# Kernel optimization log

Measured on AMD Instinct MI355X. Metric: run time of the kernel, lower is better.

Reference implementation:

```python
import jax, jax.numpy as jnp
import numpy as np


def _conv1x1(x, w, b):
    # x: (B, C, H, W), w: (O, C), b: (O,)  -> (B, O, H, W)
    return jnp.einsum('oc,bchw->bohw', w, x) + b[None, :, None, None]


def _branch(xq, xkv, wq, bq, wk, bk, wv, bv):
    B, C, H, W = xq.shape
    N = H * W
    q = _conv1x1(xq, wq, bq).reshape(B, -1, N)   # (B, d, N)
    k = _conv1x1(xkv, wk, bk).reshape(B, -1, N)  # (B, d, N)
    v = _conv1x1(xkv, wv, bv).reshape(B, C, N)   # (B, C, N)
    energy = jnp.einsum('bdi,bdj->bij', q, k)    # (B, N, N), no scale (as in source)
    attn = jax.nn.softmax(energy, axis=-1)
    out = jnp.einsum('bcj,bij->bci', v, attn)    # bmm(v, attn^T)
    return out.reshape(B, C, H, W)


def setup_inputs() -> dict:
    key = jax.random.key(0)
    ks = jax.random.split(key, 16)
    B, C, H, W = 4, 256, 64, 64
    d = C // 8
    s_in = 0.02
    inp = {
        'x1': jax.random.normal(ks[0], (B, C, H, W), jnp.float32),
        'x2': jax.random.normal(ks[1], (B, C, H, W), jnp.float32),
        'wq1': jax.random.normal(ks[2], (d, C), jnp.float32) * s_in,
        'bq1': jnp.zeros((d,), jnp.float32),
        'wk1': jax.random.normal(ks[3], (d, C), jnp.float32) * s_in,
        'bk1': jnp.zeros((d,), jnp.float32),
        'wv1': jax.random.normal(ks[4], (C, C), jnp.float32) * s_in,
        'bv1': jnp.zeros((C,), jnp.float32),
        'wq2': jax.random.normal(ks[5], (d, C), jnp.float32) * s_in,
        'bq2': jnp.zeros((d,), jnp.float32),
        'wk2': jax.random.normal(ks[6], (d, C), jnp.float32) * s_in,
        'bk2': jnp.zeros((d,), jnp.float32),
        'wv2': jax.random.normal(ks[7], (C, C), jnp.float32) * s_in,
        'bv2': jnp.zeros((C,), jnp.float32),
    }
    return inp


def reference(x1, x2, wq1, bq1, wk1, bk1, wv1, bv1, wq2, bq2, wk2, bk2, wv2, bv2):
    out1 = _branch(x1, x2, wq1, bq1, wk1, bk1, wv1, bv1)
    out2 = _branch(x1, x2, wq2, bq2, wk2, bk2, wv2, bv2)
    return x1 + x2 + out1 + out2
```

## Files before the change

kernel.cpp:

```cpp
#include <hip/hip_runtime.h>

#define N_TOK 4096
#define C_DIM 256
#define D_DIM 32

typedef float f32x4 __attribute__((ext_vector_type(4)));
typedef short short8 __attribute__((ext_vector_type(8)));
typedef unsigned short u16;

__device__ __forceinline__ u16 f2bf(float f) {
    unsigned int u = __builtin_bit_cast(unsigned int, f);
    u += 0x7fffu + ((u >> 16) & 1u);
    return (u16)(u >> 16);
}
__device__ __forceinline__ u16 f2bf_fast(float f) {
    return (u16)((__builtin_bit_cast(unsigned int, f) + 0x8000u) >> 16);
}
__device__ __forceinline__ float bf2f(u16 h) {
    unsigned int u = ((unsigned int)h) << 16;
    return __builtin_bit_cast(float, u);
}
__device__ __forceinline__ float exp2_fast(float x) {
#if __has_builtin(__builtin_amdgcn_exp2f)
    return __builtin_amdgcn_exp2f(x);
#else
    return exp2f(x);
#endif
}

__global__ __launch_bounds__(256) void qk_proj(
    const float* __restrict__ x1, const float* __restrict__ x2,
    const float* __restrict__ wq1, const float* __restrict__ bq1,
    const float* __restrict__ wk1, const float* __restrict__ bk1,
    const float* __restrict__ wq2, const float* __restrict__ bq2,
    const float* __restrict__ wk2, const float* __restrict__ bk2,
    u16* __restrict__ wsQ, u16* __restrict__ wsK)
{
    __shared__ float w_lds[32 * 256];
    const int ib = blockIdx.x;
    const int comb = blockIdx.y;
    const int b = comb & 3;
    const int branch = (comb >> 2) & 1;
    const int qk = comb >> 3;

    const float* x = qk ? x2 : x1;
    const float* w; const float* bias; u16* dst;
    if (qk == 0) { w = branch ? wq2 : wq1; bias = branch ? bq2 : bq1; dst = wsQ; }
    else         { w = branch ? wk2 : wk1; bias = branch ? bk2 : bk1; dst = wsK; }
    const int slice = branch * 4 + b;
    dst += (size_t)slice * N_TOK * D_DIM;
    const float osc = (qk == 0) ? 1.44269504088896341f : 1.0f;

    const int tid = threadIdx.x;
    for (int t = tid; t < 32 * 256; t += 256) w_lds[t] = w[t];
    __syncthreads();

    const int il = tid & 63;
    const int db = tid >> 6;
    const float* xc = x + (size_t)b * C_DIM * N_TOK + ib * 64 + il;

    float acc[8] = {0.f,0.f,0.f,0.f,0.f,0.f,0.f,0.f};
    for (int c4 = 0; c4 < 256; c4 += 4) {
        const float xv0 = xc[(size_t)(c4 + 0) * N_TOK];
        const float xv1 = xc[(size_t)(c4 + 1) * N_TOK];
        const float xv2 = xc[(size_t)(c4 + 2) * N_TOK];
        const float xv3 = xc[(size_t)(c4 + 3) * N_TOK];
#pragma unroll
        for (int mm = 0; mm < 8; ++mm) {
            const float4 wv = *(const float4*)&w_lds[(db * 8 + mm) * 256 + c4];
            acc[mm] += xv0 * wv.x + xv1 * wv.y + xv2 * wv.z + xv3 * wv.w;
        }
    }
    short8 pack;
#pragma unroll
    for (int mm = 0; mm < 8; ++mm)
        pack[mm] = (short)f2bf((acc[mm] + bias[db * 8 + mm]) * osc);
    *(short8*)(dst + (size_t)(ib * 64 + il) * D_DIM + db * 8) = pack;
}

__device__ __forceinline__ void stage_xt(u16* xtb, const float* xb, int ks,
                                         int wave, int lane)
{
    const int j  = (wave & 1) * 64 + lane;
    const int cb = (wave >> 1) * 16;
    const float* xp = xb + (size_t)(ks * 32 + cb) * N_TOK + j;
    u16 vals[16];
#pragma unroll
    for (int qq = 0; qq < 16; ++qq) vals[qq] = f2bf(xp[(size_t)qq * N_TOK]);
    const int swz = (j >> 1) & 3;
    u16* row = xtb + j * 32;
    const int c0 = cb >> 3;
    *(short8*)&row[((c0    ) ^ swz) * 8] = *(const short8*)&vals[0];
    *(short8*)&row[((c0 + 1) ^ swz) * 8] = *(const short8*)&vals[8];
}

__global__ __launch_bounds__(256, 2) void v_proj(
    const float* __restrict__ x2,
    const float* __restrict__ wv1, const float* __restrict__ bv1,
    const float* __restrict__ wv2, const float* __restrict__ bv2,
    u16* __restrict__ wsV)
{
    __shared__ __align__(16) u16 wl[128 * 256];
    __shared__ __align__(16) u16 xt[2][128 * 32];

    const int jt = blockIdx.x, ct = blockIdx.y, s = blockIdx.z;
    const int branch = s >> 2, b = s & 3;
    const float* w    = branch ? wv2 : wv1;
    const float* bias = branch ? bv2 : bv1;
    u16* dst = wsV + (size_t)s * C_DIM * N_TOK;
    const float* xb = x2 + (size_t)b * C_DIM * N_TOK + jt * 128;

    const int tid = threadIdx.x;
    const int wave = tid >> 6, lane = tid & 63;
    const int wr = wave >> 1, wc = wave & 1;
    const int g = lane >> 4, li = lane & 15;

    {
        const int c = tid >> 1;
        const int kh = (tid & 1) * 128;
        const float* wrow = w + (size_t)(ct * 128 + c) * C_DIM + kh;
        u16* lrow = wl + c * 256;
#pragma unroll
        for (int kk = 0; kk < 128; kk += 8) {
            const float4 a0 = *(const float4*)&wrow[kk];
            const float4 a1 = *(const float4*)&wrow[kk + 4];
            u16 tmp[8] = {f2bf(a0.x), f2bf(a0.y), f2bf(a0.z), f2bf(a0.w),
                          f2bf(a1.x), f2bf(a1.y), f2bf(a1.z), f2bf(a1.w)};
            const int kc = (kh + kk) >> 3;
            *(short8*)&lrow[(kc ^ (c & 7)) * 8] = *(const short8*)tmp;
        }
    }
    stage_xt(&xt[0][0], xb, 0, wave, lane);
    __syncthreads();

    f32x4 acc[4][4];
#pragma unroll
    for (int mf = 0; mf < 4; ++mf)
#pragma unroll
        for (int nf = 0; nf < 4; ++nf) acc[mf][nf] = (f32x4){0.f, 0.f, 0.f, 0.f};

    int buf = 0;
    for (int ks = 0; ks < 8; ++ks) {
        if (ks < 7) stage_xt(&xt[buf ^ 1][0], xb, ks + 1, wave, lane);

        short8 af[4], bf[4];
#pragma unroll
        for (int mf = 0; mf < 4; ++mf) {
            const int c = wr * 64 + mf * 16 + li;
            af[mf] = *(const short8*)&wl[c * 256 + (((ks * 4 + g) ^ (li & 7)) * 8)];
        }
#pragma unroll
        for (int nf = 0; nf < 4; ++nf) {
            const int j = wc * 64 + nf * 16 + li;
            bf[nf] = *(const short8*)&xt[buf][j * 32 + ((g ^ ((j >> 1) & 3)) * 8)];
        }
        __builtin_amdgcn_s_setprio(1);
#pragma unroll
        for (int mf = 0; mf < 4; ++mf)
#pragma unroll
            for (int nf = 0; nf < 4; ++nf)
                acc[mf][nf] = __builtin_amdgcn_mfma_f32_16x16x32_bf16(
                    af[mf], bf[nf], acc[mf][nf], 0, 0, 0);
        __builtin_amdgcn_s_setprio(0);
        __syncthreads();
        buf ^= 1;
    }

#pragma unroll
    for (int mf = 0; mf < 4; ++mf) {
#pragma unroll
        for (int r = 0; r < 4; ++r) {
            const int c = ct * 128 + wr * 64 + mf * 16 + 4 * g + r;
            const float bv = bias[c];
            u16* drow = dst + (size_t)c * N_TOK + jt * 128;
#pragma unroll
            for (int nf = 0; nf < 4; ++nf)
                drow[wc * 64 + nf * 16 + li] = f2bf(acc[mf][nf][r] + bv);
        }
    }
}

__device__ __forceinline__ void stage_v64(const u16* vsl, short* dst,
                                          int wg, int lane, int j0)
{
#pragma unroll
    for (int ii = 0; ii < 8; ++ii) {
        const int rbase = wg * 64 + ii * 8;
        const int row = rbase + (lane >> 3);
        const int swz = ((row >> 2) & 3) | ((row & 1) << 2);
        const int cp = (lane & 7) ^ swz;
        const u16* gp = vsl + (size_t)row * N_TOK + j0 + cp * 8;
        short* lp = dst + rbase * 64;
        __builtin_amdgcn_global_load_lds(
            (const __attribute__((address_space(1))) void*)gp,
            (__attribute__((address_space(3))) void*)lp, 16, 0, 0);
    }
}

__global__ __launch_bounds__(512, 2) void attn_fwd(
    const u16* __restrict__ Q, const u16* __restrict__ K,
    const u16* __restrict__ V, u16* __restrict__ O)
{
    __shared__ __align__(16) short vlds[2][2][256 * 64];
    __shared__ float lscr[2][4][64][2];

    const int n  = blockIdx.x;
    const int s  = n & 7;
    const int ib = n >> 3;
    const u16* q = Q + (size_t)s * N_TOK * D_DIM;
    const u16* k = K + (size_t)s * N_TOK * D_DIM;
    const u16* v = V + (size_t)s * C_DIM * N_TOK;
    u16*       o = O + (size_t)s * N_TOK * C_DIM;

    const int tid  = threadIdx.x;
    const int wave = tid >> 6;
    const int lane = tid & 63;
    const int grp  = wave >> 2;
    const int wg   = wave & 3;
    const int g    = lane >> 4;
    const int li   = lane & 15;
    const int i0   = ib * 128 + wg * 32;
    const int jbase = grp * (N_TOK / 2);
    const int NP = N_TOK / 2 / 64;

    short8 qf[2];
    qf[0] = *(const short8*)(q + (size_t)(i0 + li) * D_DIM + 8 * g);
    qf[1] = *(const short8*)(q + (size_t)(i0 + 16 + li) * D_DIM + 8 * g);

    f32x4 acc[2][16];
#pragma unroll
    for (int it = 0; it < 2; ++it)
#pragma unroll
        for (int cf = 0; cf < 16; ++cf) acc[it][cf] = (f32x4){0.f, 0.f, 0.f, 0.f};
    float lsum[2] = {0.f, 0.f};

    const int swz3 = ((li >> 2) & 3) | ((li & 1) << 2);

    short8 kf0 = *(const short8*)(k + (size_t)(jbase + 2 * li     ) * D_DIM + 8 * g);
    short8 kf1 = *(const short8*)(k + (size_t)(jbase + 2 * li + 1 ) * D_DIM + 8 * g);
    short8 kf2 = *(const short8*)(k + (size_t)(jbase + 32 + 2 * li) * D_DIM + 8 * g);
    short8 kf3 = *(const short8*)(k + (size_t)(jbase + 33 + 2 * li) * D_DIM + 8 * g);
    stage_v64(v, &vlds[grp][0][0], wg, lane, jbase);
    __syncthreads();

    int buf = 0;
    for (int p = 0; p < NP; ++p) {
        short8 kn0, kn1, kn2, kn3;
        if (p < NP - 1) {
            const int jn = jbase + (p + 1) * 64;
            kn0 = *(const short8*)(k + (size_t)(jn + 2 * li     ) * D_DIM + 8 * g);
            kn1 = *(const short8*)(k + (size_t)(jn + 2 * li + 1 ) * D_DIM + 8 * g);
            kn2 = *(const short8*)(k + (size_t)(jn + 32 + 2 * li) * D_DIM + 8 * g);
            kn3 = *(const short8*)(k + (size_t)(jn + 33 + 2 * li) * D_DIM + 8 * g);
            stage_v64(v, &vlds[grp][buf ^ 1][0], wg, lane, jn);
        }

        const f32x4 z = (f32x4){0.f, 0.f, 0.f, 0.f};
        const short* vb = &vlds[grp][buf][0];
#pragma unroll
        for (int ss = 0; ss < 2; ++ss) {
            const short8 ke = ss ? kf2 : kf0;
            const short8 ko = ss ? kf3 : kf1;
            short8 pa[2];
#pragma unroll
            for (int it = 0; it < 2; ++it) {
                f32x4 se = __builtin_amdgcn_mfma_f32_16x16x32_bf16(ke, qf[it], z, 0, 0, 0);
                f32x4 so = __builtin_amdgcn_mfma_f32_16x16x32_bf16(ko, qf[it], z, 0, 0, 0);
                float pe[4], po[4];
#pragma unroll
                for (int r = 0; r < 4; ++r) {
                    pe[r] = exp2_fast(se[r]);
                    po[r] = exp2_fast(so[r]);
                }
                lsum[it] += ((pe[0] + po[0]) + (pe[1] + po[1]))
                          + ((pe[2] + po[2]) + (pe[3] + po[3]));
#pragma unroll
                for (int r = 0; r < 4; ++r) {
                    pa[it][2 * r]     = (short)f2bf_fast(pe[r]);
                    pa[it][2 * r + 1] = (short)f2bf_fast(po[r]);
                }
            }
            __builtin_amdgcn_s_setprio(1);
#pragma unroll
            for (int cf = 0; cf < 16; ++cf) {
                const short8 vf = *(const short8*)
                    &vb[(cf * 16 + li) * 64 + ((((ss << 2) + g) ^ swz3) * 8)];
                acc[0][cf] = __builtin_amdgcn_mfma_f32_16x16x32_bf16(pa[0], vf, acc[0][cf], 0, 0, 0);
                acc[1][cf] = __builtin_amdgcn_mfma_f32_16x16x32_bf16(pa[1], vf, acc[1][cf], 0, 0, 0);
            }
            __builtin_amdgcn_s_setprio(0);
        }
        __syncthreads();
        buf ^= 1;
        if (p < NP - 1) { kf0 = kn0; kf1 = kn1; kf2 = kn2; kf3 = kn3; }
    }

#pragma unroll
    for (int it = 0; it < 2; ++it) {
        lsum[it] += __shfl_xor(lsum[it], 16);
        lsum[it] += __shfl_xor(lsum[it], 32);
        lscr[grp][wg][lane][it] = lsum[it];
    }
    __syncthreads();
    float linv[2];
#pragma unroll
    for (int it = 0; it < 2; ++it)
        linv[it] = 1.0f / (lsum[it] + lscr[grp ^ 1][wg][lane][it]);

    f32x4* pv = (f32x4*)&vlds[0][0][0];
#pragma unroll
    for (int it = 0; it < 2; ++it) {
        __syncthreads();
        if (grp == 1) {
#pragma unroll
            for (int cf = 0; cf < 16; ++cf)
                pv[(cf * 4 + wg) * 64 + lane] = acc[it][cf];
        }
        __syncthreads();
        if (grp == 0) {
#pragma unroll
            for (int cf = 0; cf < 16; ++cf) {
                const f32x4 o4 = pv[(cf * 4 + wg) * 64 + lane];
                acc[it][cf][0] += o4[0]; acc[it][cf][1] += o4[1];
                acc[it][cf][2] += o4[2]; acc[it][cf][3] += o4[3];
            }
        }
    }

    if (grp == 0) {
#pragma unroll
        for (int it = 0; it < 2; ++it) {
            float lr[4];
#pragma unroll
            for (int r = 0; r < 4; ++r) lr[r] = __shfl(linv[it], 4 * g + r);
#pragma unroll
            for (int cf = 0; cf < 16; ++cf)
#pragma unroll
                for (int r = 0; r < 4; ++r)
                    o[(size_t)(i0 + it * 16 + 4 * g + r) * C_DIM + cf * 16 + li] =
                        f2bf(acc[it][cf][r] * lr[r]);
        }
    }
}

__global__ __launch_bounds__(256) void epilogue(
    const float* __restrict__ x1, const float* __restrict__ x2,
    const u16* __restrict__ O, float* __restrict__ out)
{
    __shared__ float tl[64][65];
    const int it = blockIdx.x, ct = blockIdx.y, b = blockIdx.z;
    const int tid = threadIdx.x;
    const int cl = tid & 63, r0 = tid >> 6;

    const u16* O1 = O + (size_t)(b)     * N_TOK * C_DIM;
    const u16* O2 = O + (size_t)(4 + b) * N_TOK * C_DIM;

#pragma unroll
    for (int rr = 0; rr < 16; ++rr) {
        const int il = r0 + rr * 4;
        const size_t off = (size_t)(it * 64 + il) * C_DIM + ct * 64 + cl;
        tl[il][cl] = bf2f(O1[off]) + bf2f(O2[off]);
    }
    __syncthreads();
#pragma unroll
    for (int rr = 0; rr < 16; ++rr) {
        const int c2 = r0 + rr * 4;
        const size_t idx = ((size_t)b * C_DIM + ct * 64 + c2) * N_TOK + it * 64 + cl;
        out[idx] = x1[idx] + x2[idx] + tl[cl][c2];
    }
}

extern "C" void kernel_launch(void* const* d_in, const int* in_sizes, int n_in,
                              void* d_out, int out_size, void* d_ws, size_t ws_size,
                              hipStream_t stream)
{
    const float* x1  = (const float*)d_in[0];
    const float* x2  = (const float*)d_in[1];
    const float* wq1 = (const float*)d_in[2];
    const float* bq1 = (const float*)d_in[3];
    const float* wk1 = (const float*)d_in[4];
    const float* bk1 = (const float*)d_in[5];
    const float* wv1 = (const float*)d_in[6];
    const float* bv1 = (const float*)d_in[7];
    const float* wq2 = (const float*)d_in[8];
    const float* bq2 = (const float*)d_in[9];
    const float* wk2 = (const float*)d_in[10];
    const float* bk2 = (const float*)d_in[11];
    const float* wv2 = (const float*)d_in[12];
    const float* bv2 = (const float*)d_in[13];
    float* out = (float*)d_out;

    u16* wsQ = (u16*)d_ws;
    u16* wsK = wsQ + (size_t)8 * N_TOK * D_DIM;
    u16* wsV = wsK + (size_t)8 * N_TOK * D_DIM;
    u16* wsO = wsV + (size_t)8 * C_DIM * N_TOK;

    qk_proj<<<dim3(64, 16), 256, 0, stream>>>(x1, x2, wq1, bq1, wk1, bk1,
                                              wq2, bq2, wk2, bk2, wsQ, wsK);
    v_proj<<<dim3(32, 2, 8), 256, 0, stream>>>(x2, wv1, bv1, wv2, bv2, wsV);
    attn_fwd<<<dim3(256), 512, 0, stream>>>(wsQ, wsK, wsV, wsO);
    epilogue<<<dim3(64, 4, 4), 256, 0, stream>>>(x1, x2, wsO, out);
}
```

Before: 170.2 us.

## Split attention keys four ways with 64 query rows per wave

The attention kernel now splits the key dimension across four wave groups instead of two. Each wave handles 64 query rows (four 16-row tiles) rather than 32, and the key step drops from 64 to 32 with a new V staging swizzle. Each V fragment read from LDS now feeds four MFMAs instead of two, which cuts LDS traffic per FLOP. In exchange, each wave holds twice as many accumulators (256 floats), launch bounds fall to one block per SIMD-pair, and the cross-group reduction grows to three partial sums.

```diff
diff --git a/kernel.cpp b/kernel.cpp
--- a/kernel.cpp
+++ b/kernel.cpp
@@ -180,29 +180,28 @@
     }
 }
 
-__device__ __forceinline__ void stage_v64(const u16* vsl, short* dst,
+__device__ __forceinline__ void stage_v32(const u16* vsl, short* dst,
                                           int wg, int lane, int j0)
 {
+    const int cp = (lane & 3) ^ ((lane >> 3) & 3);
 #pragma unroll
     for (int ii = 0; ii < 8; ++ii) {
-        const int rbase = wg * 64 + ii * 8;
-        const int row = rbase + (lane >> 3);
-        const int swz = ((row >> 2) & 3) | ((row & 1) << 2);
-        const int cp = (lane & 7) ^ swz;
+        const int rbase = ii * 32 + wg * 16;
+        const int row = rbase + (lane >> 2);
         const u16* gp = vsl + (size_t)row * N_TOK + j0 + cp * 8;
-        short* lp = dst + rbase * 64;
+        short* lp = dst + rbase * 32;
         __builtin_amdgcn_global_load_lds(
             (const __attribute__((address_space(1))) void*)gp,
             (__attribute__((address_space(3))) void*)lp, 16, 0, 0);
     }
 }
 
-__global__ __launch_bounds__(512, 2) void attn_fwd(
+__global__ __launch_bounds__(512, 1) void attn_fwd(
     const u16* __restrict__ Q, const u16* __restrict__ K,
     const u16* __restrict__ V, u16* __restrict__ O)
 {
-    __shared__ __align__(16) short vlds[2][2][256 * 64];
-    __shared__ float lscr[2][4][64][2];
+    __shared__ __align__(16) short vlds[4][2][256 * 32];
+    __shared__ float lscr[4][2][64][4];
 
     const int n  = blockIdx.x;
     const int s  = n & 7;
@@ -215,124 +214,120 @@
     const int tid  = threadIdx.x;
     const int wave = tid >> 6;
     const int lane = tid & 63;
-    const int grp  = wave >> 2;
-    const int wg   = wave & 3;
+    const int grp  = wave >> 1;
+    const int wg   = wave & 1;
     const int g    = lane >> 4;
     const int li   = lane & 15;
-    const int i0   = ib * 128 + wg * 32;
-    const int jbase = grp * (N_TOK / 2);
-    const int NP = N_TOK / 2 / 64;
-
-    short8 qf[2];
-    qf[0] = *(const short8*)(q + (size_t)(i0 + li) * D_DIM + 8 * g);
-    qf[1] = *(const short8*)(q + (size_t)(i0 + 16 + li) * D_DIM + 8 * g);
-
-    f32x4 acc[2][16];
-#pragma unroll
-    for (int it = 0; it < 2; ++it)
+    const int i0   = ib * 128 + wg * 64;
+    const int jbase = grp * (N_TOK / 4);
+    const int NP = N_TOK / 4 / 32;
+
+    short8 qf[4];
+#pragma unroll
+    for (int it = 0; it < 4; ++it)
+        qf[it] = *(const short8*)(q + (size_t)(i0 + it * 16 + li) * D_DIM + 8 * g);
+
+    f32x4 acc[4][16];
+#pragma unroll
+    for (int it = 0; it < 4; ++it)
 #pragma unroll
         for (int cf = 0; cf < 16; ++cf) acc[it][cf] = (f32x4){0.f, 0.f, 0.f, 0.f};
-    float lsum[2] = {0.f, 0.f};
-
-    const int swz3 = ((li >> 2) & 3) | ((li & 1) << 2);
-
-    short8 kf0 = *(const short8*)(k + (size_t)(jbase + 2 * li     ) * D_DIM + 8 * g);
-    short8 kf1 = *(const short8*)(k + (size_t)(jbase + 2 * li + 1 ) * D_DIM + 8 * g);
-    short8 kf2 = *(const short8*)(k + (size_t)(jbase + 32 + 2 * li) * D_DIM + 8 * g);
-    short8 kf3 = *(const short8*)(k + (size_t)(jbase + 33 + 2 * li) * D_DIM + 8 * g);
-    stage_v64(v, &vlds[grp][0][0], wg, lane, jbase);
+    float lsum[4] = {0.f, 0.f, 0.f, 0.f};
+
+    const int roff = (g ^ ((li >> 1) & 3)) << 3;
+
+    short8 ke = *(const short8*)(k + (size_t)(jbase + 2 * li    ) * D_DIM + 8 * g);
+    short8 ko = *(const short8*)(k + (size_t)(jbase + 2 * li + 1) * D_DIM + 8 * g);
+    stage_v32(v, &vlds[grp][0][0], wg, lane, jbase);
     __syncthreads();
 
     int buf = 0;
     for (int p = 0; p < NP; ++p) {
-        short8 kn0, kn1, kn2, kn3;
+        short8 kne, kno;
         if (p < NP - 1) {
-            const int jn = jbase + (p + 1) * 64;
-            kn0 = *(const short8*)(k + (size_t)(jn + 2 * li     ) * D_DIM + 8 * g);
-            kn1 = *(const short8*)(k + (size_t)(jn + 2 * li + 1 ) * D_DIM + 8 * g);
-            kn2 = *(const short8*)(k + (size_t)(jn + 32 + 2 * li) * D_DIM + 8 * g);
-            kn3 = *(const short8*)(k + (size_t)(jn + 33 + 2 * li) * D_DIM + 8 * g);
-            stage_v64(v, &vlds[grp][buf ^ 1][0], wg, lane, jn);
+            const int jn = jbase + (p + 1) * 32;
+            kne = *(const short8*)(k + (size_t)(jn + 2 * li    ) * D_DIM + 8 * g);
+            kno = *(const short8*)(k + (size_t)(jn + 2 * li + 1) * D_DIM + 8 * g);
+            stage_v32(v, &vlds[grp][buf ^ 1][0], wg, lane, jn);
         }
 
         const f32x4 z = (f32x4){0.f, 0.f, 0.f, 0.f};
+        short8 pa[4];
+#pragma unroll
+        for (int it = 0; it < 4; ++it) {
+            f32x4 se = __builtin_amdgcn_mfma_f32_16x16x32_bf16(ke, qf[it], z, 0, 0, 0);
+            f32x4 so = __builtin_amdgcn_mfma_f32_16x16x32_bf16(ko, qf[it], z, 0, 0, 0);
+            float pe[4], po[4];
+#pragma unroll
+            for (int r = 0; r < 4; ++r) {
+                pe[r] = exp2_fast(se[r]);
+                po[r] = exp2_fast(so[r]);
+            }
+            lsum[it] += ((pe[0] + po[0]) + (pe[1] + po[1]))
+                      + ((pe[2] + po[2]) + (pe[3] + po[3]));
+#pragma unroll
+            for (int r = 0; r < 4; ++r) {
+                pa[it][2 * r]     = (short)f2bf_fast(pe[r]);
+                pa[it][2 * r + 1] = (short)f2bf_fast(po[r]);
+            }
+        }
+
         const short* vb = &vlds[grp][buf][0];
-#pragma unroll
-        for (int ss = 0; ss < 2; ++ss) {
-            const short8 ke = ss ? kf2 : kf0;
-            const short8 ko = ss ? kf3 : kf1;
-            short8 pa[2];
-#pragma unroll
-            for (int it = 0; it < 2; ++it) {
-                f32x4 se = __builtin_amdgcn_mfma_f32_16x16x32_bf16(ke, qf[it], z, 0, 0, 0);
-                f32x4 so = __builtin_amdgcn_mfma_f32_16x16x32_bf16(ko, qf[it], z, 0, 0, 0);
-                float pe[4], po[4];
-#pragma unroll
-                for (int r = 0; r < 4; ++r) {
-                    pe[r] = exp2_fast(se[r]);
-                    po[r] = exp2_fast(so[r]);
-                }
-                lsum[it] += ((pe[0] + po[0]) + (pe[1] + po[1]))
-                          + ((pe[2] + po[2]) + (pe[3] + po[3]));
-#pragma unroll
-                for (int r = 0; r < 4; ++r) {
-                    pa[it][2 * r]     = (short)f2bf_fast(pe[r]);
-                    pa[it][2 * r + 1] = (short)f2bf_fast(po[r]);
-                }
-            }
-            __builtin_amdgcn_s_setprio(1);
-#pragma unroll
-            for (int cf = 0; cf < 16; ++cf) {
-                const short8 vf = *(const short8*)
-                    &vb[(cf * 16 + li) * 64 + ((((ss << 2) + g) ^ swz3) * 8)];
-                acc[0][cf] = __builtin_amdgcn_mfma_f32_16x16x32_bf16(pa[0], vf, acc[0][cf], 0, 0, 0);
-                acc[1][cf] = __builtin_amdgcn_mfma_f32_16x16x32_bf16(pa[1], vf, acc[1][cf], 0, 0, 0);
-            }
-            __builtin_amdgcn_s_setprio(0);
-        }
+        __builtin_amdgcn_s_setprio(1);
+#pragma unroll
+        for (int cf = 0; cf < 16; ++cf) {
+            const short8 vf = *(const short8*)&vb[(cf * 16 + li) * 32 + roff];
+            acc[0][cf] = __builtin_amdgcn_mfma_f32_16x16x32_bf16(pa[0], vf, acc[0][cf], 0, 0, 0);
+            acc[1][cf] = __builtin_amdgcn_mfma_f32_16x16x32_bf16(pa[1], vf, acc[1][cf], 0, 0, 0);
+            acc[2][cf] = __builtin_amdgcn_mfma_f32_16x16x32_bf16(pa[2], vf, acc[2][cf], 0, 0, 0);
+            acc[3][cf] = __builtin_amdgcn_mfma_f32_16x16x32_bf16(pa[3], vf, acc[3][cf], 0, 0, 0);
+        }
+        __builtin_amdgcn_s_setprio(0);
         __syncthreads();
         buf ^= 1;
-        if (p < NP - 1) { kf0 = kn0; kf1 = kn1; kf2 = kn2; kf3 = kn3; }
-    }
-
-#pragma unroll
-    for (int it = 0; it < 2; ++it) {
+        if (p < NP - 1) { ke = kne; ko = kno; }
+    }
+
+#pragma unroll
+    for (int it = 0; it < 4; ++it) {
         lsum[it] += __shfl_xor(lsum[it], 16);
         lsum[it] += __shfl_xor(lsum[it], 32);
         lscr[grp][wg][lane][it] = lsum[it];
     }
-    __syncthreads();
-    float linv[2];
-#pragma unroll
-    for (int it = 0; it < 2; ++it)
-        linv[it] = 1.0f / (lsum[it] + lscr[grp ^ 1][wg][lane][it]);
 
     f32x4* pv = (f32x4*)&vlds[0][0][0];
 #pragma unroll
-    for (int it = 0; it < 2; ++it) {
+    for (int it = 0; it < 4; ++it) {
         __syncthreads();
-        if (grp == 1) {
+        if (grp != 0) {
+            const int base = ((grp - 1) * 2 + wg) * 1024;
 #pragma unroll
             for (int cf = 0; cf < 16; ++cf)
-                pv[(cf * 4 + wg) * 64 + lane] = acc[it][cf];
+                pv[base + cf * 64 + lane] = acc[it][cf];
         }
         __syncthreads();
         if (grp == 0) {
 #pragma unroll
-            for (int cf = 0; cf < 16; ++cf) {
-                const f32x4 o4 = pv[(cf * 4 + wg) * 64 + lane];
-                acc[it][cf][0] += o4[0]; acc[it][cf][1] += o4[1];
-                acc[it][cf][2] += o4[2]; acc[it][cf][3] += o4[3];
+            for (int sg = 0; sg < 3; ++sg) {
+                const int base = (sg * 2 + wg) * 1024;
+#pragma unroll
+                for (int cf = 0; cf < 16; ++cf) {
+                    const f32x4 o4 = pv[base + cf * 64 + lane];
+                    acc[it][cf][0] += o4[0]; acc[it][cf][1] += o4[1];
+                    acc[it][cf][2] += o4[2]; acc[it][cf][3] += o4[3];
+                }
             }
         }
     }
 
     if (grp == 0) {
 #pragma unroll
-        for (int it = 0; it < 2; ++it) {
+        for (int it = 0; it < 4; ++it) {
+            const float linv = 1.0f / (lscr[0][wg][lane][it] + lscr[1][wg][lane][it]
+                                     + lscr[2][wg][lane][it] + lscr[3][wg][lane][it]);
             float lr[4];
 #pragma unroll
-            for (int r = 0; r < 4; ++r) lr[r] = __shfl(linv[it], 4 * g + r);
+            for (int r = 0; r < 4; ++r) lr[r] = __shfl(linv, 4 * g + r);
 #pragma unroll
             for (int cf = 0; cf < 16; ++cf)
 #pragma unroll
```

Result: slower. 570.6 us (+235.3%).
